# Performance work log

Measured on AMD Instinct MI355X. Metric: run time of the kernel, lower is better.

Reference implementation:

```python
import jax, jax.numpy as jnp
import numpy as np

D = 1024

def setup_inputs() -> dict:
    key = jax.random.key(0)
    ks = jax.random.split(key, 7)
    s = 1.0 / np.sqrt(D)
    return {
        "x": jax.random.normal(ks[0], (8, 2048, D), dtype=jnp.float32),
        "Wq": jax.random.uniform(ks[1], (D, D), jnp.float32, -s, s),
        "bq": jax.random.uniform(ks[2], (D,), jnp.float32, -s, s),
        "Wk": jax.random.uniform(ks[3], (D, D), jnp.float32, -s, s),
        "bk": jax.random.uniform(ks[4], (D,), jnp.float32, -s, s),
        "Wv": jax.random.uniform(ks[5], (D, D), jnp.float32, -s, s),
        "bv": jax.random.uniform(ks[6], (D,), jnp.float32, -s, s),
    }

def reference(x, Wq, bq, Wk, bk, Wv, bv):
    # torch Linear: y = x @ W.T + b
    Q = jnp.einsum('bsd,ed->bse', x, Wq) + bq
    K = jnp.einsum('bsd,ed->bse', x, Wk) + bk
    V = jnp.einsum('bsd,ed->bse', x, Wv) + bv
    scores = jnp.einsum('bse,bte->bst', Q, K) / jnp.sqrt(jnp.float32(x.shape[-1]))
    weights = jax.nn.softmax(scores, axis=-1)
    out = jnp.einsum('bst,bte->bse', weights, V)
    return jnp.mean(out, axis=0)
```

## Files before the change

kernel.cpp:

```cpp
#include <hip/hip_runtime.h>

typedef unsigned short u16;
typedef __attribute__((ext_vector_type(8))) short s16x8;
typedef __attribute__((ext_vector_type(4))) short s16x4;
typedef __attribute__((ext_vector_type(4))) float f32x4;

typedef const __attribute__((address_space(1))) void gas_void;
typedef __attribute__((address_space(3))) void las_void;

__device__ inline u16 f2bf(float f){
  union { float f; unsigned u; } c; c.f = f;
  unsigned r = c.u + 0x7fffu + ((c.u >> 16) & 1u);
  return (u16)(r >> 16);
}
__device__ inline float bf2f(u16 b){
  union { unsigned u; float f; } c; c.u = ((unsigned)b) << 16;
  return c.f;
}

extern "C" __global__ __launch_bounds__(256) void cvt_f32_bf16(
    const float* __restrict__ src, u16* __restrict__ dst, int n4){
  int stride = gridDim.x * blockDim.x;
  for (int i = blockIdx.x * blockDim.x + threadIdx.x; i < n4; i += stride){
    float4 f = reinterpret_cast<const float4*>(src)[i];
    s16x4 o;
    o[0] = (short)f2bf(f.x); o[1] = (short)f2bf(f.y);
    o[2] = (short)f2bf(f.z); o[3] = (short)f2bf(f.w);
    reinterpret_cast<s16x4*>(dst)[i] = o;
  }
}

extern "C" __global__ __launch_bounds__(256) void cvt_w3(
    const float* __restrict__ w0, const float* __restrict__ w1,
    const float* __restrict__ w2, u16* __restrict__ dst, int n4each){
  int stride = gridDim.x * blockDim.x;
  int total = 3 * n4each;
  for (int i = blockIdx.x * blockDim.x + threadIdx.x; i < total; i += stride){
    int w = i / n4each, off = i - w * n4each;
    const float* src = w == 0 ? w0 : w == 1 ? w1 : w2;
    float4 f = reinterpret_cast<const float4*>(src)[off];
    s16x4 o;
    o[0] = (short)f2bf(f.x); o[1] = (short)f2bf(f.y);
    o[2] = (short)f2bf(f.z); o[3] = (short)f2bf(f.w);
    reinterpret_cast<s16x4*>(dst)[i] = o;
  }
}

extern "C" __global__ __launch_bounds__(256) void reduce8(
    const float* __restrict__ p, float* __restrict__ out, int n4, long stride4){
  int gs = gridDim.x * blockDim.x;
  for (int i = blockIdx.x * blockDim.x + threadIdx.x; i < n4; i += gs){
    float4 a = reinterpret_cast<const float4*>(p)[i];
    #pragma unroll
    for (int z = 1; z < 8; ++z){
      float4 b = reinterpret_cast<const float4*>(p)[i + z * stride4];
      a.x += b.x; a.y += b.y; a.z += b.z; a.w += b.w;
    }
    reinterpret_cast<float4*>(out)[i] = a;
  }
}

#define BM 256
#define BN 256
#define BK 64

__device__ inline void stage256(const u16* __restrict__ g, int ld, int row0, int k0,
                                u16* lds, int tid){
  const int wave = tid >> 6;
  #pragma unroll
  for (int j = 0; j < 4; ++j){
    int c = j * 512 + tid;
    int row = c >> 3, sch = c & 7;
    int ch = sch ^ (row & 7);
    const u16* src = g + (long)(row0 + row) * ld + k0 + ch * 8;
    u16* dst = lds + (size_t)(j * 512 + wave * 64) * 8;
    __builtin_amdgcn_global_load_lds((gas_void*)src, (las_void*)dst, 16, 0, 0);
  }
}

#define BARRIER() do { asm volatile("" ::: "memory"); \
                       __builtin_amdgcn_s_barrier();  \
                       asm volatile("" ::: "memory"); } while (0)

#define MFMA16(RO) do { __builtin_amdgcn_s_setprio(1);                         \
    _Pragma("unroll")                                                          \
    for (int i_ = 0; i_ < 4; ++i_)                                             \
      _Pragma("unroll")                                                        \
      for (int j_ = 0; j_ < 4; ++j_)                                           \
        acc[(RO) + i_][j_] = __builtin_amdgcn_mfma_f32_16x16x32_bf16(          \
            af[i_], bfr[j_], acc[(RO) + i_][j_], 0, 0, 0);                     \
    __builtin_amdgcn_s_setprio(0); } while (0)

template<int EPI>
__global__ __launch_bounds__(512, 2) void gemm256(
    const u16* __restrict__ A, const u16* __restrict__ B, void* __restrict__ C,
    const float* __restrict__ bias, float scale, int K,
    int lda, int ldb, int ldc, long sAz, long sBz, long sCz)
{
  __shared__ u16 As[2][BM * BK];
  __shared__ u16 Bs[2][BN * BK];
  const int tid = threadIdx.x;
  const int lane = tid & 63, wave = tid >> 6;
  const int wm = (wave >> 2) * 128, wn = (wave & 3) * 64;

  const int gx = gridDim.x;
  const int nwg = gx * gridDim.y;
  const int hw = blockIdx.y * gx + blockIdx.x;
  const int lg = (hw & 7) * (nwg >> 3) + (hw >> 3);
  const int pr  = lg / (2 * gx);
  const int rem = lg - pr * 2 * gx;
  const int bm = (pr * 2 + (rem & 1)) * BM;
  const int bn = (rem >> 1) * BN;
  const int z = blockIdx.z;
  A += (long)z * sAz; B += (long)z * sBz;

  f32x4 acc[8][4];
  #pragma unroll
  for (int i = 0; i < 8; ++i)
    #pragma unroll
    for (int j = 0; j < 4; ++j) acc[i][j] = (f32x4){0.f, 0.f, 0.f, 0.f};

  const int lrow = lane & 15, lkg = lane >> 4;
  const int nt = K >> 6;

  auto lda4 = [&](s16x8* d, const u16* base, int ih, int kk){
    #pragma unroll
    for (int i = 0; i < 4; ++i){
      int row = wm + (ih * 4 + i) * 16 + lrow;
      int ch = (kk * 4 + lkg) ^ (row & 7);
      d[i] = *reinterpret_cast<const s16x8*>(
          reinterpret_cast<const char*>(base) + row * 128 + ch * 16);
    }
  };
  auto ldb4 = [&](s16x8* d, const u16* base, int kk){
    #pragma unroll
    for (int j = 0; j < 4; ++j){
      int row = wn + j * 16 + lrow;
      int ch = (kk * 4 + lkg) ^ (row & 7);
      d[j] = *reinterpret_cast<const s16x8*>(
          reinterpret_cast<const char*>(base) + row * 128 + ch * 16);
    }
  };

  stage256(A, lda, bm, 0, As[0], tid);
  stage256(B, ldb, bn, 0, Bs[0], tid);
  asm volatile("s_waitcnt vmcnt(0)" ::: "memory");
  BARRIER();

  for (int t = 0; t < nt; ++t){
    const int cur = t & 1, nxt = cur ^ 1;
    const bool pf = (t + 1) < nt;
    const int k1 = (t + 1) << 6;
    const u16* as = As[cur];
    const u16* bs = Bs[cur];
    s16x8 af[4], bfr[4];

    ldb4(bfr, bs, 0);
    lda4(af, as, 0, 0);
    if (pf) stage256(A, lda, bm, k1, As[nxt], tid);
    BARRIER();
    MFMA16(0);
    BARRIER();

    lda4(af, as, 1, 0);
    if (pf) stage256(B, ldb, bn, k1, Bs[nxt], tid);
    BARRIER();
    MFMA16(4);
    BARRIER();

    ldb4(bfr, bs, 1);
    lda4(af, as, 0, 1);
    BARRIER();
    MFMA16(0);
    BARRIER();

    lda4(af, as, 1, 1);
    if (pf) asm volatile("s_waitcnt vmcnt(0)" ::: "memory");
    BARRIER();
    MFMA16(4);
    BARRIER();
  }

  #pragma unroll
  for (int i = 0; i < 8; ++i){
    #pragma unroll
    for (int j = 0; j < 4; ++j){
      #pragma unroll
      for (int r = 0; r < 4; ++r){
        int row = bm + wm + i * 16 + lkg * 4 + r;
        int col = bn + wn + j * 16 + lrow;
        float v = acc[i][j][r] * scale;
        if (EPI == 0){
          if (bias) v += bias[col];
          reinterpret_cast<u16*>(C)[(long)z * sCz + (long)row * ldc + col] = f2bf(v);
        } else if (EPI == 1){
          if (bias) v += bias[col];
          int b = row >> 11, tt = row & 2047;
          reinterpret_cast<u16*>(C)[((long)b << 21) + ((long)col << 11) + tt] = f2bf(v);
        } else {
          reinterpret_cast<float*>(C)[(long)z * sCz + (long)row * ldc + col] = v;
        }
      }
    }
  }
}

extern "C" __global__ __launch_bounds__(256) void softmax_rows(u16* __restrict__ S){
  long row = blockIdx.x;
  u16* p = S + row * 2048;
  int tid = threadIdx.x;
  s16x8 vv = reinterpret_cast<s16x8*>(p)[tid];
  float v[8];
  float m = -3.4e38f;
  #pragma unroll
  for (int j = 0; j < 8; ++j){ v[j] = bf2f((u16)vv[j]); m = fmaxf(m, v[j]); }
  #pragma unroll
  for (int o = 32; o; o >>= 1) m = fmaxf(m, __shfl_xor(m, o));
  __shared__ float sm[4], ss[4];
  int wave = tid >> 6, lane = tid & 63;
  if (lane == 0) sm[wave] = m;
  __syncthreads();
  m = fmaxf(fmaxf(sm[0], sm[1]), fmaxf(sm[2], sm[3]));
  float e[8], s = 0.f;
  #pragma unroll
  for (int j = 0; j < 8; ++j){ e[j] = __expf(v[j] - m); s += e[j]; }
  #pragma unroll
  for (int o = 32; o; o >>= 1) s += __shfl_xor(s, o);
  if (lane == 0) ss[wave] = s;
  __syncthreads();
  s = ss[0] + ss[1] + ss[2] + ss[3];
  float inv = 1.0f / s;
  s16x8 ov;
  #pragma unroll
  for (int j = 0; j < 8; ++j) ov[j] = (short)f2bf(e[j] * inv);
  reinterpret_cast<s16x8*>(p)[tid] = ov;
}

extern "C" void kernel_launch(void* const* d_in, const int* in_sizes, int n_in,
                              void* d_out, int out_size, void* d_ws, size_t ws_size,
                              hipStream_t stream){
  const float* x  = (const float*)d_in[0];
  const float* Wq = (const float*)d_in[1];
  const float* bq = (const float*)d_in[2];
  const float* Wk = (const float*)d_in[3];
  const float* bk = (const float*)d_in[4];
  const float* Wv = (const float*)d_in[5];
  const float* bv = (const float*)d_in[6];

  const long NX = 16384L * 1024;
  const long NW = 1024L * 1024;
  const long NS = 8L * 2048 * 2048;

  u16* xbf = (u16*)d_ws;
  u16* Wb  = xbf + NX;
  u16* Qb  = Wb + 3 * NW;
  u16* Kb  = Qb + NX;
  u16* Vtb = Kb + NX;
  u16* S   = Vtb + NX;

  float* partial = (float*)Qb;

  size_t need = (size_t)(NX + 3 * NW + 3 * NX + NS) * 2;
  if (ws_size < need) return;

  cvt_f32_bf16<<<2048, 256, 0, stream>>>(x, xbf, (int)(NX / 4));
  cvt_w3<<<768, 256, 0, stream>>>(Wq, Wk, Wv, Wb, (int)(NW / 4));

  gemm256<0><<<dim3(4, 64, 1), 512, 0, stream>>>(
      xbf, Wb,          Qb,  bq, 1.f, 1024, 1024, 1024, 1024, 0, 0, 0);
  gemm256<0><<<dim3(4, 64, 1), 512, 0, stream>>>(
      xbf, Wb + NW,     Kb,  bk, 1.f, 1024, 1024, 1024, 1024, 0, 0, 0);
  gemm256<1><<<dim3(4, 64, 1), 512, 0, stream>>>(
      xbf, Wb + 2 * NW, Vtb, bv, 1.f, 1024, 1024, 1024, 0,    0, 0, 0);

  gemm256<0><<<dim3(8, 8, 8), 512, 0, stream>>>(
      Qb, Kb, S, nullptr, 0.03125f, 1024, 1024, 1024, 2048,
      2048L * 1024, 2048L * 1024, 2048L * 2048);

  softmax_rows<<<8 * 2048, 256, 0, stream>>>(S);

  gemm256<2><<<dim3(4, 8, 8), 512, 0, stream>>>(
      S, Vtb, partial, nullptr, 0.125f, 2048, 2048, 2048, 1024,
      2048L * 2048, 1024L * 2048, 2048L * 1024);

  reduce8<<<1024, 256, 0, stream>>>(
      partial, (float*)d_out, (int)(2048L * 1024 / 4), 2048L * 1024 / 4);
}
```

Baseline: 360.4 us.

## Cut per-iteration GEMM barriers with double fragment registers; wave-per-row softmax

The GEMM main loop now keeps two sets of A and B fragment registers, so LDS reads for the next sub-step run ahead of the MFMAs. This removes the seven intra-iteration barriers and leaves a single wait and barrier at the end of each K tile. The softmax is rewritten so that one wave handles a whole 2048-wide row with shuffle-only reductions in a grid-stride persistent loop, which eliminates shared-memory reductions and __syncthreads. The cost is more live registers in the GEMM, and possibly less overlap when global_load_lds writes into the other LDS buffer while reads proceed without barriers.

```diff
diff --git a/kernel.cpp b/kernel.cpp
--- a/kernel.cpp
+++ b/kernel.cpp
@@ -82,15 +82,6 @@
                        __builtin_amdgcn_s_barrier();  \
                        asm volatile("" ::: "memory"); } while (0)
 
-#define MFMA16(RO) do { __builtin_amdgcn_s_setprio(1);                         \
-    _Pragma("unroll")                                                          \
-    for (int i_ = 0; i_ < 4; ++i_)                                             \
-      _Pragma("unroll")                                                        \
-      for (int j_ = 0; j_ < 4; ++j_)                                           \
-        acc[(RO) + i_][j_] = __builtin_amdgcn_mfma_f32_16x16x32_bf16(          \
-            af[i_], bfr[j_], acc[(RO) + i_][j_], 0, 0, 0);                     \
-    __builtin_amdgcn_s_setprio(0); } while (0)
-
 template<int EPI>
 __global__ __launch_bounds__(512, 2) void gemm256(
     const u16* __restrict__ A, const u16* __restrict__ B, void* __restrict__ C,
@@ -142,6 +133,14 @@
     }
   };
 
+  #define MFMACL(AF, BF, RO)                                                   \
+    _Pragma("unroll")                                                          \
+    for (int i_ = 0; i_ < 4; ++i_)                                             \
+      _Pragma("unroll")                                                        \
+      for (int j_ = 0; j_ < 4; ++j_)                                           \
+        acc[(RO) + i_][j_] = __builtin_amdgcn_mfma_f32_16x16x32_bf16(          \
+            AF[i_], BF[j_], acc[(RO) + i_][j_], 0, 0, 0);
+
   stage256(A, lda, bm, 0, As[0], tid);
   stage256(B, ldb, bn, 0, Bs[0], tid);
   asm volatile("s_waitcnt vmcnt(0)" ::: "memory");
@@ -153,31 +152,28 @@
     const int k1 = (t + 1) << 6;
     const u16* as = As[cur];
     const u16* bs = Bs[cur];
-    s16x8 af[4], bfr[4];
-
-    ldb4(bfr, bs, 0);
-    lda4(af, as, 0, 0);
+    s16x8 af0[4], af1[4], bfr0[4], bfr1[4];
+
+    ldb4(bfr0, bs, 0);
+    lda4(af0, as, 0, 0);
+    lda4(af1, as, 1, 0);
+    __builtin_amdgcn_s_setprio(1);
+    MFMACL(af0, bfr0, 0);
+    __builtin_amdgcn_s_setprio(0);
+    ldb4(bfr1, bs, 1);
+    lda4(af0, as, 0, 1);
     if (pf) stage256(A, lda, bm, k1, As[nxt], tid);
-    BARRIER();
-    MFMA16(0);
-    BARRIER();
-
-    lda4(af, as, 1, 0);
+    __builtin_amdgcn_s_setprio(1);
+    MFMACL(af1, bfr0, 4);
+    __builtin_amdgcn_s_setprio(0);
+    lda4(af1, as, 1, 1);
     if (pf) stage256(B, ldb, bn, k1, Bs[nxt], tid);
-    BARRIER();
-    MFMA16(4);
-    BARRIER();
-
-    ldb4(bfr, bs, 1);
-    lda4(af, as, 0, 1);
-    BARRIER();
-    MFMA16(0);
-    BARRIER();
-
-    lda4(af, as, 1, 1);
-    if (pf) asm volatile("s_waitcnt vmcnt(0)" ::: "memory");
-    BARRIER();
-    MFMA16(4);
+    __builtin_amdgcn_s_setprio(1);
+    MFMACL(af0, bfr1, 0);
+    MFMACL(af1, bfr1, 4);
+    __builtin_amdgcn_s_setprio(0);
+
+    asm volatile("s_waitcnt vmcnt(0)" ::: "memory");
     BARRIER();
   }
 
@@ -203,37 +199,43 @@
       }
     }
   }
-}
-
-extern "C" __global__ __launch_bounds__(256) void softmax_rows(u16* __restrict__ S){
-  long row = blockIdx.x;
-  u16* p = S + row * 2048;
-  int tid = threadIdx.x;
-  s16x8 vv = reinterpret_cast<s16x8*>(p)[tid];
-  float v[8];
-  float m = -3.4e38f;
-  #pragma unroll
-  for (int j = 0; j < 8; ++j){ v[j] = bf2f((u16)vv[j]); m = fmaxf(m, v[j]); }
-  #pragma unroll
-  for (int o = 32; o; o >>= 1) m = fmaxf(m, __shfl_xor(m, o));
-  __shared__ float sm[4], ss[4];
-  int wave = tid >> 6, lane = tid & 63;
-  if (lane == 0) sm[wave] = m;
-  __syncthreads();
-  m = fmaxf(fmaxf(sm[0], sm[1]), fmaxf(sm[2], sm[3]));
-  float e[8], s = 0.f;
-  #pragma unroll
-  for (int j = 0; j < 8; ++j){ e[j] = __expf(v[j] - m); s += e[j]; }
-  #pragma unroll
-  for (int o = 32; o; o >>= 1) s += __shfl_xor(s, o);
-  if (lane == 0) ss[wave] = s;
-  __syncthreads();
-  s = ss[0] + ss[1] + ss[2] + ss[3];
-  float inv = 1.0f / s;
-  s16x8 ov;
-  #pragma unroll
-  for (int j = 0; j < 8; ++j) ov[j] = (short)f2bf(e[j] * inv);
-  reinterpret_cast<s16x8*>(p)[tid] = ov;
+  #undef MFMACL
+}
+
+extern "C" __global__ __launch_bounds__(512) void softmax_rows_w(
+    u16* __restrict__ S, int rows){
+  const int lane = threadIdx.x & 63;
+  const int gw = blockIdx.x * (blockDim.x >> 6) + (threadIdx.x >> 6);
+  const int nw = gridDim.x * (blockDim.x >> 6);
+  for (int row = gw; row < rows; row += nw){
+    u16* p = S + (long)row * 2048;
+    float v[32];
+    float m = -3.4e38f;
+    #pragma unroll
+    for (int c = 0; c < 4; ++c){
+      s16x8 vv = reinterpret_cast<const s16x8*>(p)[c * 64 + lane];
+      #pragma unroll
+      for (int j = 0; j < 8; ++j){
+        float f = bf2f((u16)vv[c * 0 + j]);
+        v[c * 8 + j] = f; m = fmaxf(m, f);
+      }
+    }
+    #pragma unroll
+    for (int o = 32; o; o >>= 1) m = fmaxf(m, __shfl_xor(m, o));
+    float s = 0.f;
+    #pragma unroll
+    for (int j = 0; j < 32; ++j){ v[j] = __expf(v[j] - m); s += v[j]; }
+    #pragma unroll
+    for (int o = 32; o; o >>= 1) s += __shfl_xor(s, o);
+    float inv = 1.0f / s;
+    #pragma unroll
+    for (int c = 0; c < 4; ++c){
+      s16x8 ov;
+      #pragma unroll
+      for (int j = 0; j < 8; ++j) ov[j] = (short)f2bf(v[c * 8 + j] * inv);
+      reinterpret_cast<s16x8*>(p)[c * 64 + lane] = ov;
+    }
+  }
 }
 
 extern "C" void kernel_launch(void* const* d_in, const int* in_sizes, int n_in,
@@ -277,7 +279,7 @@
       Qb, Kb, S, nullptr, 0.03125f, 1024, 1024, 1024, 2048,
       2048L * 1024, 2048L * 1024, 2048L * 2048);
 
-  softmax_rows<<<8 * 2048, 256, 0, stream>>>(S);
+  softmax_rows_w<<<256, 512, 0, stream>>>(S, 8 * 2048);
 
   gemm256<2><<<dim3(4, 8, 8), 512, 0, stream>>>(
       S, Vtb, partial, nullptr, 0.125f, 2048, 2048, 2048, 1024,
```

Result: faster. 339.3 us (-5.9%).
